# Kernel tuning notes

Measured on AMD Instinct MI355X. Metric: run time of the kernel, lower is better.

Reference implementation:

```python
import jax, jax.numpy as jnp
import numpy as np

B, L, D_E = 2, 2048, 1024
H, D_Q = 16, 64
EPS = 1e-5


def setup_inputs() -> dict:
    key = jax.random.key(0)
    ks = jax.random.split(key, 12)
    s_in = 1.0 / np.sqrt(D_E)
    s_mid = 1.0 / np.sqrt(H * D_Q)
    return {
        "pre_q": jax.random.normal(ks[0], (B, L, D_E), jnp.float32),
        "pre_k": jax.random.normal(ks[1], (B, L, D_E), jnp.float32),
        "Wq": jax.random.normal(ks[2], (D_E, H * D_Q), jnp.float32) * s_in,
        "bq": jnp.zeros((H * D_Q,), jnp.float32),
        "Wk": jax.random.normal(ks[3], (D_E, H * D_Q), jnp.float32) * s_in,
        "bk": jnp.zeros((H * D_Q,), jnp.float32),
        "Wv": jax.random.normal(ks[4], (D_E, H * D_Q), jnp.float32) * s_in,
        "bv": jnp.zeros((H * D_Q,), jnp.float32),
        "Wo": jax.random.normal(ks[5], (H * D_Q, D_E), jnp.float32) * s_mid,
        "bo": jnp.zeros((D_E,), jnp.float32),
        "gamma": jnp.ones((D_E,), jnp.float32),
        "beta": jnp.zeros((D_E,), jnp.float32),
    }


def reference(pre_q, pre_k, Wq, bq, Wk, bk, Wv, bv, Wo, bo, gamma, beta):
    b, ql, _ = pre_q.shape
    kl = pre_k.shape[1]
    q = (pre_q @ Wq + bq).reshape(b, ql, H, D_Q)
    k = (pre_k @ Wk + bk).reshape(b, kl, H, D_Q)
    v = (pre_k @ Wv + bv).reshape(b, kl, H, D_Q)
    scores = jnp.einsum('bqhd,bkhd->bhqk', q, k) / jnp.sqrt(jnp.float32(D_Q))
    attn = jax.nn.softmax(scores, axis=-1)
    ctx = jnp.einsum('bhqk,bkhd->bqhd', attn, v).reshape(b, ql, H * D_Q)
    out = ctx @ Wo + bo
    x = pre_q + out
    mu = jnp.mean(x, axis=-1, keepdims=True)
    var = jnp.mean(jnp.square(x - mu), axis=-1, keepdims=True)
    return (x - mu) * jax.lax.rsqrt(var + EPS) * gamma + beta
```

## Files before the change

kernel.cpp:

```cpp
#include <hip/hip_runtime.h>
#include <hip/hip_bf16.h>
#include <cstdint>

typedef unsigned short ushort_t;
typedef __attribute__((ext_vector_type(8))) short short8;
typedef __attribute__((ext_vector_type(8))) __bf16 bf16x8;
typedef __attribute__((ext_vector_type(4))) float f32x4;
typedef __attribute__((ext_vector_type(4))) ushort_t ushort4v;
typedef __attribute__((ext_vector_type(2))) unsigned int uint2v;
typedef __attribute__((ext_vector_type(4))) unsigned int uint4v;

__device__ inline ushort_t f2bf(float f) {
    union { float f; unsigned u; } x; x.f = f;
    unsigned r = x.u + 0x7fffu + ((x.u >> 16) & 1u);
    return (ushort_t)(r >> 16);
}

__device__ inline unsigned pkbf(float a, float b) {
    __hip_bfloat162 h = __float22bfloat162_rn(float2{a, b});
    unsigned r;
    __builtin_memcpy(&r, &h, 4);
    return r;
}

__device__ inline float bf2f(ushort_t u) {
    unsigned v = (unsigned)u << 16;
    return __builtin_bit_cast(float, v);
}

__device__ inline unsigned pktrunc(float a, float b) {
    return __builtin_amdgcn_perm(__builtin_bit_cast(unsigned, b),
                                 __builtin_bit_cast(unsigned, a), 0x07060302u);
}

#if __has_builtin(__builtin_amdgcn_exp2f)
#define EXP2(x) __builtin_amdgcn_exp2f(x)
#else
#define EXP2(x) __builtin_exp2f(x)
#endif

__device__ inline bf16x8 ldfrag(const ushort_t* p) {
    short8 s = *(const short8*)p;
    return __builtin_bit_cast(bf16x8, s);
}

__device__ inline f32x4 mfma16(bf16x8 a, bf16x8 b, f32x4 c) {
    return __builtin_amdgcn_mfma_f32_16x16x32_bf16(a, b, c, 0, 0, 0);
}

__device__ inline void glds16(const ushort_t* g, ushort_t* l) {
    __builtin_amdgcn_global_load_lds((const __attribute__((address_space(1))) void*)g,
                                     (__attribute__((address_space(3))) void*)l, 16, 0, 0);
}

__global__ __launch_bounds__(256) void prep_k(const float* __restrict__ W0, const float* __restrict__ W1,
                                              const float* __restrict__ W2, const float* __restrict__ W3,
                                              ushort_t* __restrict__ wout) {
    const int blk = blockIdx.x;
    const int t = threadIdx.x;
    const int z = blk >> 10;
    const int bx = (blk & 31) * 32, by = ((blk >> 5) & 31) * 32;
    const float* W = (z == 0) ? W0 : (z == 1) ? W1 : (z == 2) ? W2 : W3;
    ushort_t* o = wout + (size_t)z * (1u << 20);
    __shared__ float tile[32][33];
    const int tx = t & 31, ty = t >> 5;
#pragma unroll
    for (int r = 0; r < 4; ++r)
        tile[ty + r * 8][tx] = W[(size_t)(by + ty + r * 8) * 1024 + bx + tx];
    __syncthreads();
#pragma unroll
    for (int r = 0; r < 4; ++r)
        o[(size_t)(bx + ty + r * 8) * 1024 + by + tx] = f2bf(tile[tx][ty + r * 8]);
}

template <int MODE>
__global__ __launch_bounds__(256) void gemm128(
    const float* __restrict__ Af1, const float* __restrict__ Af2,
    const ushort_t* __restrict__ A1,
    const ushort_t* __restrict__ Wt,
    const float* __restrict__ bias0, const float* __restrict__ bias1, const float* __restrict__ bias2,
    ushort_t* __restrict__ oQ, ushort_t* __restrict__ oK, ushort_t* __restrict__ oVt,
    const float* __restrict__ resid, ushort_t* __restrict__ oXb) {
    const int t = threadIdx.x;
    const int phys = blockIdx.x;
    const int bid = (MODE == 0) ? (phys & 7) * 96 + (phys >> 3)
                                : (phys & 7) * 32 + (phys >> 3);
    int g, mb, nb;
    const float* bias;
    const ushort_t* Wg;
    if (MODE == 0) {
        g = bid >> 8;
        const int rem = bid & 255;
        mb = rem >> 3;
        nb = rem & 7;
        Wg = Wt + (size_t)g * (1u << 20);
        bias = (g == 0) ? bias0 : (g == 1) ? bias1 : bias2;
    } else {
        g = 0;
        mb = bid >> 3;
        nb = bid & 7;
        Wg = Wt;
        bias = bias0;
    }
    const int m0 = mb * 128, n0 = nb * 128;

    __shared__ ushort_t As[3][128 * 32];
    __shared__ ushort_t Bs[3][128 * 32];
    const int row4 = t >> 2, c8 = (t & 3) * 8;
    const ushort_t* Bg = Wg + (size_t)(n0 + row4) * 1024 + c8;
    const int ldst = row4 * 32 + c8;

    const float* Agf = nullptr;
    const ushort_t* Ag = nullptr;
    if (MODE == 0)
        Agf = ((g == 0) ? Af1 : Af2) + (size_t)(m0 + row4) * 1024 + c8;
    else
        Ag = A1 + (size_t)(m0 + row4) * 1024 + c8;

    const int lane = t & 63, wid = t >> 6;
    const int wm = wid >> 1, wn = wid & 1;
    const int lr = lane & 15, lgp = lane >> 4, lk = lgp * 8;

    f32x4 acc[4][4];
#pragma unroll
    for (int j = 0; j < 4; ++j) {
        const f32x4 bj = *(const f32x4*)(bias + n0 + wn * 64 + j * 16 + 4 * lgp);
#pragma unroll
        for (int i = 0; i < 4; ++i) acc[j][i] = bj;
    }

    f32x4 a0, a1, a2, a3;

#define A_LOAD(kt)                                              \
    {                                                           \
        a0 = *(const f32x4*)(Agf + (kt));                       \
        a1 = *(const f32x4*)(Agf + (kt) + 4);                   \
        a2 = *(const f32x4*)(Agf + (kt) + 64 * 1024);           \
        a3 = *(const f32x4*)(Agf + (kt) + 64 * 1024 + 4);       \
    }

#define A_WRITE(buf)                                                               \
    {                                                                              \
        uint4v w0 = {pkbf(a0[0], a0[1]), pkbf(a0[2], a0[3]),                       \
                     pkbf(a1[0], a1[1]), pkbf(a1[2], a1[3])};                      \
        *(uint4v*)&As[buf][ldst] = w0;                                             \
        uint4v w1 = {pkbf(a2[0], a2[1]), pkbf(a2[2], a2[3]),                       \
                     pkbf(a3[0], a3[1]), pkbf(a3[2], a3[3])};                      \
        *(uint4v*)&As[buf][ldst + 2048] = w1;                                      \
    }

#define B_STAGE(buf, kt)                                        \
    {                                                           \
        glds16(Bg + (kt), &Bs[buf][ldst]);                      \
        glds16(Bg + (kt) + 64 * 1024, &Bs[buf][ldst + 2048]);   \
    }

#define A_STAGE_G(buf, kt)                                      \
    {                                                           \
        glds16(Ag + (kt), &As[buf][ldst]);                      \
        glds16(Ag + (kt) + 64 * 1024, &As[buf][ldst + 2048]);   \
    }

#define COMPUTE(buf)                                                              \
    {                                                                             \
        bf16x8 af[4], bfr[4];                                                     \
        _Pragma("unroll") for (int i = 0; i < 4; ++i)                             \
            af[i] = ldfrag(&As[buf][(wm * 64 + i * 16 + lr) * 32 + lk]);          \
        _Pragma("unroll") for (int j = 0; j < 4; ++j)                             \
            bfr[j] = ldfrag(&Bs[buf][(wn * 64 + j * 16 + lr) * 32 + lk]);         \
        __builtin_amdgcn_s_setprio(1);                                            \
        _Pragma("unroll") for (int j = 0; j < 4; ++j)                             \
            _Pragma("unroll") for (int i = 0; i < 4; ++i)                         \
                acc[j][i] = mfma16(bfr[j], af[i], acc[j][i]);                     \
        __builtin_amdgcn_s_setprio(0);                                            \
    }

#define GITER0(it, buf, buf2)                                                     \
    {                                                                             \
        if ((it) <= 30) { asm volatile("s_waitcnt vmcnt(2)" ::: "memory"); }      \
        else            { asm volatile("s_waitcnt vmcnt(0)" ::: "memory"); }      \
        A_WRITE(buf)                                                              \
        __syncthreads();                                                          \
        if ((it) + 1 < 32) A_LOAD(((it) + 1) * 32)                                \
        if ((it) + 2 < 32) B_STAGE(buf2, ((it) + 2) * 32)                         \
        COMPUTE(buf)                                                              \
    }

#define GITER1(it, buf, buf2)                                                     \
    {                                                                             \
        if ((it) <= 30) { asm volatile("s_waitcnt vmcnt(4)" ::: "memory"); }      \
        else            { asm volatile("s_waitcnt vmcnt(0)" ::: "memory"); }      \
        __syncthreads();                                                          \
        if ((it) + 2 < 32) { A_STAGE_G(buf2, ((it) + 2) * 32) B_STAGE(buf2, ((it) + 2) * 32) } \
        COMPUTE(buf)                                                              \
    }

    if (MODE == 0) {
        B_STAGE(0, 0);
        A_LOAD(0);
        B_STAGE(1, 32);
        for (int b3 = 0; b3 < 30; b3 += 3) {
            GITER0(b3 + 0, 0, 2)
            GITER0(b3 + 1, 1, 0)
            GITER0(b3 + 2, 2, 1)
        }
        GITER0(30, 0, 2)
        GITER0(31, 1, 0)
    } else {
        A_STAGE_G(0, 0) B_STAGE(0, 0);
        A_STAGE_G(1, 32) B_STAGE(1, 32);
        for (int b3 = 0; b3 < 30; b3 += 3) {
            GITER1(b3 + 0, 0, 2)
            GITER1(b3 + 1, 1, 0)
            GITER1(b3 + 2, 2, 1)
        }
        GITER1(30, 0, 2)
        GITER1(31, 1, 0)
    }
#undef A_LOAD
#undef A_WRITE
#undef B_STAGE
#undef A_STAGE_G
#undef COMPUTE
#undef GITER0
#undef GITER1

    const float qs = (MODE == 0 && g == 0) ? 0.18033688011f : 1.0f;

#pragma unroll
    for (int j = 0; j < 4; ++j) {
        const int n = n0 + wn * 64 + j * 16 + 4 * lgp;
#pragma unroll
        for (int i = 0; i < 4; ++i) {
            const f32x4 v = acc[j][i];
            const int m = m0 + wm * 64 + i * 16 + lr;
            if (MODE == 0) {
                const int b = m >> 11, ll = m & 2047;
                const int h = n >> 6, d = n & 63;
                if (g == 2) {
                    const int lp = (ll & ~63) | (ll & 32) | (((ll >> 2) & 3) << 3)
                                 | (((ll >> 4) & 1) << 2) | (ll & 3);
#pragma unroll
                    for (int jj = 0; jj < 4; ++jj)
                        oVt[((size_t)(b * 16 + h) * 64 + d + jj) * 2048 + lp] = f2bf(v[jj]);
                } else {
                    uint2v cw = {pkbf(v[0] * qs, v[1] * qs), pkbf(v[2] * qs, v[3] * qs)};
                    ushort_t* dst = (g == 0) ? oQ : oK;
                    *(uint2v*)(dst + (((size_t)(b * 16 + h) * 2048) + ll) * 64 + d) = cw;
                }
            } else {
                const float4 r = *(const float4*)(resid + (size_t)m * 1024 + n);
                uint2v cw = {pkbf(v[0] + r.x, v[1] + r.y), pkbf(v[2] + r.z, v[3] + r.w)};
                *(uint2v*)(oXb + (size_t)m * 1024 + n) = cw;
            }
        }
    }
}

__global__ __launch_bounds__(256, 2) void attn_k(const ushort_t* __restrict__ Qg, const ushort_t* __restrict__ Kg,
                                                 const ushort_t* __restrict__ Vtg, ushort_t* __restrict__ Cg) {
    __shared__ ushort_t Ks[2][8 * 512];
    __shared__ ushort_t Vs[2][8 * 512];

    const int t = threadIdx.x;
    const int lane = t & 63, w = t >> 6;
    const int bid = blockIdx.x;
    const int xcd = bid & 7, j = bid >> 3;
    const int bh = (xcd << 2) | (j >> 4);
    const int qb = j & 15;
    const int q0 = qb * 128 + w * 32;
    const int lr = lane & 15, g = lane >> 4;
    const int srow = lane & 15, sch = lane >> 4;

    const ushort_t* Kbase = Kg + (size_t)bh * (2048 * 64);
    const ushort_t* Vbase = Vtg + (size_t)bh * (64 * 2048);

    const ushort_t* QpA = Qg + ((size_t)bh * 2048 + q0 + lr) * 64 + g * 8;
    const bf16x8 qA0 = ldfrag(QpA), qA1 = ldfrag(QpA + 32);
    const bf16x8 qB0 = ldfrag(QpA + 16 * 64), qB1 = ldfrag(QpA + 16 * 64 + 32);

    f32x4 oA[4] = {}, oB[4] = {};
    float lA = 0.f, lB = 0.f;

#define STAGE(buf, kt)                                                                        \
    {                                                                                         \
        glds16(Kbase + (size_t)((kt) + 16 * w + srow) * 64 + sch * 8, &Ks[buf][w * 512 + lane * 8]);            \
        glds16(Kbase + (size_t)((kt) + 16 * w + srow) * 64 + 32 + sch * 8, &Ks[buf][(4 + w) * 512 + lane * 8]); \
        glds16(Vbase + (size_t)(16 * w + srow) * 2048 + (kt) + sch * 8, &Vs[buf][(2 * w) * 512 + lane * 8]);    \
        glds16(Vbase + (size_t)(16 * w + srow) * 2048 + (kt) + 32 + sch * 8, &Vs[buf][(2 * w + 1) * 512 + lane * 8]); \
    }

#define COMPUTE(BUF)                                                                      \
    {                                                                                     \
        f32x4 stA[4], stB[4];                                                             \
        _Pragma("unroll") for (int f = 0; f < 4; ++f) {                                   \
            const bf16x8 k0 = ldfrag(&Ks[BUF][f * 512 + lane * 8]);                       \
            const bf16x8 k1 = ldfrag(&Ks[BUF][(4 + f) * 512 + lane * 8]);                 \
            f32x4 sA = {}, sB = {};                                                       \
            sA = mfma16(k0, qA0, sA);                                                     \
            sA = mfma16(k1, qA1, sA);                                                     \
            sB = mfma16(k0, qB0, sB);                                                     \
            sB = mfma16(k1, qB1, sB);                                                     \
            stA[f] = sA;                                                                  \
            stB[f] = sB;                                                                  \
        }                                                                                 \
        unsigned pkA[8], pkB[8];                                                          \
        float rsA = 0.f, rsB = 0.f;                                                       \
        _Pragma("unroll") for (int f = 0; f < 4; ++f) {                                   \
            const float a0 = EXP2(stA[f][0]);                                             \
            const float a1 = EXP2(stA[f][1]);                                             \
            const float a2 = EXP2(stA[f][2]);                                             \
            const float a3 = EXP2(stA[f][3]);                                             \
            rsA += (a0 + a1) + (a2 + a3);                                                 \
            pkA[2 * f] = pktrunc(a0, a1);                                                 \
            pkA[2 * f + 1] = pktrunc(a2, a3);                                             \
            const float b0 = EXP2(stB[f][0]);                                             \
            const float b1 = EXP2(stB[f][1]);                                             \
            const float b2 = EXP2(stB[f][2]);                                             \
            const float b3 = EXP2(stB[f][3]);                                             \
            rsB += (b0 + b1) + (b2 + b3);                                                 \
            pkB[2 * f] = pktrunc(b0, b1);                                                 \
            pkB[2 * f + 1] = pktrunc(b2, b3);                                             \
        }                                                                                 \
        lA += rsA;                                                                        \
        lB += rsB;                                                                        \
        _Pragma("unroll") for (int b = 0; b < 2; ++b) {                                   \
            const uint4v ua = {pkA[4 * b], pkA[4 * b + 1], pkA[4 * b + 2], pkA[4 * b + 3]}; \
            const uint4v ub = {pkB[4 * b], pkB[4 * b + 1], pkB[4 * b + 2], pkB[4 * b + 3]}; \
            const bf16x8 pA = __builtin_bit_cast(bf16x8, ua);                             \
            const bf16x8 pB = __builtin_bit_cast(bf16x8, ub);                             \
            _Pragma("unroll") for (int df = 0; df < 4; ++df) {                            \
                const bf16x8 vf = ldfrag(&Vs[BUF][(2 * df + b) * 512 + (g * 16 + lr) * 8]); \
                oA[df] = mfma16(vf, pA, oA[df]);                                          \
                oB[df] = mfma16(vf, pB, oB[df]);                                          \
            }                                                                             \
        }                                                                                 \
    }

    STAGE(0, 0);
    asm volatile("s_waitcnt vmcnt(0)" ::: "memory");
    __syncthreads();

    for (int kt2 = 0; kt2 < 2048; kt2 += 128) {
        STAGE(1, kt2 + 64);
        COMPUTE(0)
        asm volatile("s_waitcnt vmcnt(0)" ::: "memory");
        __syncthreads();
        if (kt2 + 128 < 2048) STAGE(0, kt2 + 128);
        COMPUTE(1)
        asm volatile("s_waitcnt vmcnt(0)" ::: "memory");
        __syncthreads();
    }
#undef STAGE
#undef COMPUTE

    lA += __shfl_xor(lA, 16, 64);
    lA += __shfl_xor(lA, 32, 64);
    lB += __shfl_xor(lB, 16, 64);
    lB += __shfl_xor(lB, 32, 64);

    const int bb = bh >> 4, hh = bh & 15;
    {
        const float inv = 1.0f / lA;
        ushort_t* cp = Cg + ((size_t)(bb * 2048 + q0 + lr) * 1024) + hh * 64;
#pragma unroll
        for (int df = 0; df < 4; ++df) {
            uint2v cw = {pkbf(oA[df][0] * inv, oA[df][1] * inv), pkbf(oA[df][2] * inv, oA[df][3] * inv)};
            *(uint2v*)(cp + 16 * df + 4 * g) = cw;
        }
    }
    {
        const float inv = 1.0f / lB;
        ushort_t* cp = Cg + ((size_t)(bb * 2048 + q0 + 16 + lr) * 1024) + hh * 64;
#pragma unroll
        for (int df = 0; df < 4; ++df) {
            uint2v cw = {pkbf(oB[df][0] * inv, oB[df][1] * inv), pkbf(oB[df][2] * inv, oB[df][3] * inv)};
            *(uint2v*)(cp + 16 * df + 4 * g) = cw;
        }
    }
}

__global__ __launch_bounds__(256) void ln_k(const ushort_t* __restrict__ X, const float* __restrict__ gamma,
                                            const float* __restrict__ beta, float* __restrict__ out) {
    const int row = blockIdx.x, t = threadIdx.x;
    const ushort4v xr = ((const ushort4v*)(X + (size_t)row * 1024))[t];
    const float x0 = bf2f(xr[0]), x1 = bf2f(xr[1]), x2 = bf2f(xr[2]), x3 = bf2f(xr[3]);
    float s = (x0 + x1) + (x2 + x3);
    float s2 = (x0 * x0 + x1 * x1) + (x2 * x2 + x3 * x3);
#pragma unroll
    for (int m = 1; m < 64; m <<= 1) {
        s += __shfl_xor(s, m, 64);
        s2 += __shfl_xor(s2, m, 64);
    }
    __shared__ float rs[4], rq[4];
    if ((t & 63) == 0) { rs[t >> 6] = s; rq[t >> 6] = s2; }
    __syncthreads();
    const float S = rs[0] + rs[1] + rs[2] + rs[3];
    const float S2 = rq[0] + rq[1] + rq[2] + rq[3];
    const float mu = S * (1.0f / 1024.0f);
    const float var = S2 * (1.0f / 1024.0f) - mu * mu;
    const float r = rsqrtf(var + 1e-5f);
    const float4 gg = ((const float4*)gamma)[t];
    const float4 bb = ((const float4*)beta)[t];
    float4 o;
    o.x = (x0 - mu) * r * gg.x + bb.x;
    o.y = (x1 - mu) * r * gg.y + bb.y;
    o.z = (x2 - mu) * r * gg.z + bb.z;
    o.w = (x3 - mu) * r * gg.w + bb.w;
    ((float4*)(out + (size_t)row * 1024))[t] = o;
}

extern "C" void kernel_launch(void* const* d_in, const int* in_sizes, int n_in,
                              void* d_out, int out_size, void* d_ws, size_t ws_size,
                              hipStream_t stream) {
    (void)in_sizes; (void)n_in; (void)out_size; (void)ws_size;
    const float* pre_q = (const float*)d_in[0];
    const float* pre_k = (const float*)d_in[1];
    const float* Wq = (const float*)d_in[2];
    const float* bq = (const float*)d_in[3];
    const float* Wk = (const float*)d_in[4];
    const float* bk = (const float*)d_in[5];
    const float* Wv = (const float*)d_in[6];
    const float* bv = (const float*)d_in[7];
    const float* Wo = (const float*)d_in[8];
    const float* bo = (const float*)d_in[9];
    const float* gamma = (const float*)d_in[10];
    const float* beta = (const float*)d_in[11];
    float* out = (float*)d_out;
    char* ws = (char*)d_ws;
    const size_t MB = 1024 * 1024;
    ushort_t* Wt = (ushort_t*)(ws + 16 * MB);
    ushort_t* Qb = (ushort_t*)(ws + 24 * MB);
    ushort_t* Kb = (ushort_t*)(ws + 32 * MB);
    ushort_t* Vt = (ushort_t*)(ws + 40 * MB);
    ushort_t* CTX = (ushort_t*)(ws + 48 * MB);
    ushort_t* Xres = (ushort_t*)(ws);

    prep_k<<<4096, 256, 0, stream>>>(Wq, Wk, Wv, Wo, Wt);
    gemm128<0><<<768, 256, 0, stream>>>(pre_q, pre_k, nullptr, Wt, bq, bk, bv,
                                        Qb, Kb, Vt, nullptr, nullptr);
    attn_k<<<512, 256, 0, stream>>>(Qb, Kb, Vt, CTX);
    gemm128<1><<<256, 256, 0, stream>>>(nullptr, nullptr, CTX, Wt + 3 * (1u << 20), bo, nullptr, nullptr,
                                        nullptr, nullptr, nullptr, pre_q, Xres);
    ln_k<<<4096, 256, 0, stream>>>(Xres, gamma, beta, out);
}
```

Baseline: 124.4 us.

## Deepen fp32 A prefetch and swap MFMA operands for packed V-transpose stores

In the fp32-input projection GEMM, A tiles are now prefetched two iterations ahead using two alternating register sets, so the wait count is relaxed and global-load latency has more time to hide. For the V projection, the MFMA operand order is swapped so each lane holds four consecutive sequence positions for one feature column. This lets the transposed V output be written as packed 8-byte stores instead of four scattered 2-byte stores. The cost is extra registers for the second A buffer, which may add pressure, and separate code paths per projection.

```diff
diff --git a/kernel.cpp b/kernel.cpp
--- a/kernel.cpp
+++ b/kernel.cpp
@@ -122,108 +122,178 @@
     const int lr = lane & 15, lgp = lane >> 4, lk = lgp * 8;
 
     f32x4 acc[4][4];
-#pragma unroll
-    for (int j = 0; j < 4; ++j) {
-        const f32x4 bj = *(const f32x4*)(bias + n0 + wn * 64 + j * 16 + 4 * lgp);
-#pragma unroll
-        for (int i = 0; i < 4; ++i) acc[j][i] = bj;
-    }
-
-    f32x4 a0, a1, a2, a3;
-
-#define A_LOAD(kt)                                              \
+    f32x4 aA0, aA1, aA2, aA3;
+    f32x4 aB0, aB1, aB2, aB3;
+
+#define A_LOAD0(kt)                                             \
     {                                                           \
-        a0 = *(const f32x4*)(Agf + (kt));                       \
-        a1 = *(const f32x4*)(Agf + (kt) + 4);                   \
-        a2 = *(const f32x4*)(Agf + (kt) + 64 * 1024);           \
-        a3 = *(const f32x4*)(Agf + (kt) + 64 * 1024 + 4);       \
-    }
-
-#define A_WRITE(buf)                                                               \
+        aA0 = *(const f32x4*)(Agf + (kt));                      \
+        aA1 = *(const f32x4*)(Agf + (kt) + 4);                  \
+        aA2 = *(const f32x4*)(Agf + (kt) + 64 * 1024);          \
+        aA3 = *(const f32x4*)(Agf + (kt) + 64 * 1024 + 4);      \
+    }
+#define A_LOAD1(kt)                                             \
+    {                                                           \
+        aB0 = *(const f32x4*)(Agf + (kt));                      \
+        aB1 = *(const f32x4*)(Agf + (kt) + 4);                  \
+        aB2 = *(const f32x4*)(Agf + (kt) + 64 * 1024);          \
+        aB3 = *(const f32x4*)(Agf + (kt) + 64 * 1024 + 4);      \
+    }
+#define A_WRITE0(buf)                                                              \
     {                                                                              \
-        uint4v w0 = {pkbf(a0[0], a0[1]), pkbf(a0[2], a0[3]),                       \
-                     pkbf(a1[0], a1[1]), pkbf(a1[2], a1[3])};                      \
+        uint4v w0 = {pkbf(aA0[0], aA0[1]), pkbf(aA0[2], aA0[3]),                   \
+                     pkbf(aA1[0], aA1[1]), pkbf(aA1[2], aA1[3])};                  \
         *(uint4v*)&As[buf][ldst] = w0;                                             \
-        uint4v w1 = {pkbf(a2[0], a2[1]), pkbf(a2[2], a2[3]),                       \
-                     pkbf(a3[0], a3[1]), pkbf(a3[2], a3[3])};                      \
+        uint4v w1 = {pkbf(aA2[0], aA2[1]), pkbf(aA2[2], aA2[3]),                   \
+                     pkbf(aA3[0], aA3[1]), pkbf(aA3[2], aA3[3])};                  \
         *(uint4v*)&As[buf][ldst + 2048] = w1;                                      \
     }
-
+#define A_WRITE1(buf)                                                              \
+    {                                                                              \
+        uint4v w0 = {pkbf(aB0[0], aB0[1]), pkbf(aB0[2], aB0[3]),                   \
+                     pkbf(aB1[0], aB1[1]), pkbf(aB1[2], aB1[3])};                  \
+        *(uint4v*)&As[buf][ldst] = w0;                                             \
+        uint4v w1 = {pkbf(aB2[0], aB2[1]), pkbf(aB2[2], aB2[3]),                   \
+                     pkbf(aB3[0], aB3[1]), pkbf(aB3[2], aB3[3])};                  \
+        *(uint4v*)&As[buf][ldst + 2048] = w1;                                      \
+    }
 #define B_STAGE(buf, kt)                                        \
     {                                                           \
         glds16(Bg + (kt), &Bs[buf][ldst]);                      \
         glds16(Bg + (kt) + 64 * 1024, &Bs[buf][ldst + 2048]);   \
     }
-
 #define A_STAGE_G(buf, kt)                                      \
     {                                                           \
         glds16(Ag + (kt), &As[buf][ldst]);                      \
         glds16(Ag + (kt) + 64 * 1024, &As[buf][ldst + 2048]);   \
     }
 
-#define COMPUTE(buf)                                                              \
+#define LOADFRAGS(buf)                                                            \
+    bf16x8 af[4], bfr[4];                                                         \
+    _Pragma("unroll") for (int i = 0; i < 4; ++i)                                 \
+        af[i] = ldfrag(&As[buf][(wm * 64 + i * 16 + lr) * 32 + lk]);              \
+    _Pragma("unroll") for (int j = 0; j < 4; ++j)                                 \
+        bfr[j] = ldfrag(&Bs[buf][(wn * 64 + j * 16 + lr) * 32 + lk]);
+
+#define COMPUTE_SW(buf)                                                           \
     {                                                                             \
-        bf16x8 af[4], bfr[4];                                                     \
-        _Pragma("unroll") for (int i = 0; i < 4; ++i)                             \
-            af[i] = ldfrag(&As[buf][(wm * 64 + i * 16 + lr) * 32 + lk]);          \
-        _Pragma("unroll") for (int j = 0; j < 4; ++j)                             \
-            bfr[j] = ldfrag(&Bs[buf][(wn * 64 + j * 16 + lr) * 32 + lk]);         \
+        LOADFRAGS(buf)                                                            \
         __builtin_amdgcn_s_setprio(1);                                            \
         _Pragma("unroll") for (int j = 0; j < 4; ++j)                             \
             _Pragma("unroll") for (int i = 0; i < 4; ++i)                         \
                 acc[j][i] = mfma16(bfr[j], af[i], acc[j][i]);                     \
         __builtin_amdgcn_s_setprio(0);                                            \
     }
-
-#define GITER0(it, buf, buf2)                                                     \
+#define COMPUTE_NS(buf)                                                           \
     {                                                                             \
-        if ((it) <= 30) { asm volatile("s_waitcnt vmcnt(2)" ::: "memory"); }      \
+        LOADFRAGS(buf)                                                            \
+        __builtin_amdgcn_s_setprio(1);                                            \
+        _Pragma("unroll") for (int i = 0; i < 4; ++i)                             \
+            _Pragma("unroll") for (int j = 0; j < 4; ++j)                         \
+                acc[i][j] = mfma16(af[i], bfr[j], acc[i][j]);                     \
+        __builtin_amdgcn_s_setprio(0);                                            \
+    }
+
+#define G0(it, buf, buf2, AW, AL, CMP)                                            \
+    {                                                                             \
+        if ((it) <= 30) { asm volatile("s_waitcnt vmcnt(6)" ::: "memory"); }      \
         else            { asm volatile("s_waitcnt vmcnt(0)" ::: "memory"); }      \
-        A_WRITE(buf)                                                              \
+        AW(buf)                                                                   \
         __syncthreads();                                                          \
-        if ((it) + 1 < 32) A_LOAD(((it) + 1) * 32)                                \
-        if ((it) + 2 < 32) B_STAGE(buf2, ((it) + 2) * 32)                         \
-        COMPUTE(buf)                                                              \
-    }
-
-#define GITER1(it, buf, buf2)                                                     \
+        if ((it) + 2 < 32) { AL(((it) + 2) * 32) B_STAGE(buf2, ((it) + 2) * 32) } \
+        CMP(buf)                                                                  \
+    }
+
+#define G0LOOP(CMP)                                                               \
+    A_LOAD0(0);                                                                   \
+    B_STAGE(0, 0);                                                                \
+    A_LOAD1(32);                                                                  \
+    B_STAGE(1, 32);                                                               \
+    for (int b6 = 0; b6 < 30; b6 += 6) {                                          \
+        G0(b6 + 0, 0, 2, A_WRITE0, A_LOAD0, CMP)                                  \
+        G0(b6 + 1, 1, 0, A_WRITE1, A_LOAD1, CMP)                                  \
+        G0(b6 + 2, 2, 1, A_WRITE0, A_LOAD0, CMP)                                  \
+        G0(b6 + 3, 0, 2, A_WRITE1, A_LOAD1, CMP)                                  \
+        G0(b6 + 4, 1, 0, A_WRITE0, A_LOAD0, CMP)                                  \
+        G0(b6 + 5, 2, 1, A_WRITE1, A_LOAD1, CMP)                                  \
+    }                                                                             \
+    G0(30, 0, 2, A_WRITE0, A_LOAD0, CMP)                                          \
+    G0(31, 1, 0, A_WRITE1, A_LOAD1, CMP)
+
+#define G1(it, buf, buf2)                                                         \
     {                                                                             \
         if ((it) <= 30) { asm volatile("s_waitcnt vmcnt(4)" ::: "memory"); }      \
         else            { asm volatile("s_waitcnt vmcnt(0)" ::: "memory"); }      \
         __syncthreads();                                                          \
         if ((it) + 2 < 32) { A_STAGE_G(buf2, ((it) + 2) * 32) B_STAGE(buf2, ((it) + 2) * 32) } \
-        COMPUTE(buf)                                                              \
-    }
-
-    if (MODE == 0) {
-        B_STAGE(0, 0);
-        A_LOAD(0);
-        B_STAGE(1, 32);
-        for (int b3 = 0; b3 < 30; b3 += 3) {
-            GITER0(b3 + 0, 0, 2)
-            GITER0(b3 + 1, 1, 0)
-            GITER0(b3 + 2, 2, 1)
-        }
-        GITER0(30, 0, 2)
-        GITER0(31, 1, 0)
+        COMPUTE_SW(buf)                                                           \
+    }
+
+    if (MODE == 0 && g != 2) {
+#pragma unroll
+        for (int j = 0; j < 4; ++j) {
+            const f32x4 bj = *(const f32x4*)(bias + n0 + wn * 64 + j * 16 + 4 * lgp);
+#pragma unroll
+            for (int i = 0; i < 4; ++i) acc[j][i] = bj;
+        }
+        G0LOOP(COMPUTE_SW)
+    } else if (MODE == 0) {
+        float bn[4];
+#pragma unroll
+        for (int j = 0; j < 4; ++j) bn[j] = bias[n0 + wn * 64 + j * 16 + lr];
+#pragma unroll
+        for (int i = 0; i < 4; ++i)
+#pragma unroll
+            for (int j = 0; j < 4; ++j) acc[i][j] = (f32x4){bn[j], bn[j], bn[j], bn[j]};
+        G0LOOP(COMPUTE_NS)
     } else {
+#pragma unroll
+        for (int j = 0; j < 4; ++j) {
+            const f32x4 bj = *(const f32x4*)(bias + n0 + wn * 64 + j * 16 + 4 * lgp);
+#pragma unroll
+            for (int i = 0; i < 4; ++i) acc[j][i] = bj;
+        }
         A_STAGE_G(0, 0) B_STAGE(0, 0);
         A_STAGE_G(1, 32) B_STAGE(1, 32);
         for (int b3 = 0; b3 < 30; b3 += 3) {
-            GITER1(b3 + 0, 0, 2)
-            GITER1(b3 + 1, 1, 0)
-            GITER1(b3 + 2, 2, 1)
-        }
-        GITER1(30, 0, 2)
-        GITER1(31, 1, 0)
-    }
-#undef A_LOAD
-#undef A_WRITE
+            G1(b3 + 0, 0, 2)
+            G1(b3 + 1, 1, 0)
+            G1(b3 + 2, 2, 1)
+        }
+        G1(30, 0, 2)
+        G1(31, 1, 0)
+    }
+#undef A_LOAD0
+#undef A_LOAD1
+#undef A_WRITE0
+#undef A_WRITE1
 #undef B_STAGE
 #undef A_STAGE_G
-#undef COMPUTE
-#undef GITER0
-#undef GITER1
+#undef LOADFRAGS
+#undef COMPUTE_SW
+#undef COMPUTE_NS
+#undef G0
+#undef G0LOOP
+#undef G1
+
+    if (MODE == 0 && g == 2) {
+#pragma unroll
+        for (int j = 0; j < 4; ++j) {
+            const int n = n0 + wn * 64 + j * 16 + lr;
+            const int h = n >> 6, d = n & 63;
+#pragma unroll
+            for (int i = 0; i < 4; ++i) {
+                const f32x4 v = acc[i][j];
+                const int m = m0 + wm * 64 + i * 16 + lgp * 4;
+                const int b = m >> 11, ll = m & 2047;
+                const int lp = (ll & ~63) | (ll & 32) | (((ll >> 2) & 3) << 3)
+                             | (((ll >> 4) & 1) << 2);
+                uint2v cw = {pkbf(v[0], v[1]), pkbf(v[2], v[3])};
+                *(uint2v*)(oVt + ((size_t)(b * 16 + h) * 64 + d) * 2048 + lp) = cw;
+            }
+        }
+        return;
+    }
 
     const float qs = (MODE == 0 && g == 0) ? 0.18033688011f : 1.0f;
 
@@ -237,17 +307,9 @@
             if (MODE == 0) {
                 const int b = m >> 11, ll = m & 2047;
                 const int h = n >> 6, d = n & 63;
-                if (g == 2) {
-                    const int lp = (ll & ~63) | (ll & 32) | (((ll >> 2) & 3) << 3)
-                                 | (((ll >> 4) & 1) << 2) | (ll & 3);
-#pragma unroll
-                    for (int jj = 0; jj < 4; ++jj)
-                        oVt[((size_t)(b * 16 + h) * 64 + d + jj) * 2048 + lp] = f2bf(v[jj]);
-                } else {
-                    uint2v cw = {pkbf(v[0] * qs, v[1] * qs), pkbf(v[2] * qs, v[3] * qs)};
-                    ushort_t* dst = (g == 0) ? oQ : oK;
-                    *(uint2v*)(dst + (((size_t)(b * 16 + h) * 2048) + ll) * 64 + d) = cw;
-                }
+                uint2v cw = {pkbf(v[0] * qs, v[1] * qs), pkbf(v[2] * qs, v[3] * qs)};
+                ushort_t* dst = (g == 0) ? oQ : oK;
+                *(uint2v*)(dst + (((size_t)(b * 16 + h) * 2048) + ll) * 64 + d) = cw;
             } else {
                 const float4 r = *(const float4*)(resid + (size_t)m * 1024 + n);
                 uint2v cw = {pkbf(v[0] + r.x, v[1] + r.y), pkbf(v[2] + r.z, v[3] + r.w)};
```

New measurement: 143.8 us. 1.16x slower.
